# Optimization experiments

Measured on AMD Instinct MI355X. Metric: run time of the kernel, lower is better.

Reference implementation:

```python
import jax, jax.numpy as jnp
import numpy as np

B, N, IN_DIM, D, P, C = 256, 2048, 2, 128, 2048, 10
LN_EPS = 1e-5
NORM_EPS = 1e-12


def setup_inputs() -> dict:
    key = jax.random.key(0)
    ks = jax.random.split(key, 9)
    X = jax.random.normal(ks[0], (B, N, IN_DIM), dtype=jnp.float32)
    # deterministic pair subsample (stands in for torch.combinations + randperm[:max_pairs])
    rng = np.random.default_rng(0)
    i = rng.integers(0, N, size=(P,))
    j = rng.integers(0, N, size=(P,))
    j = np.where(i == j, (j + 1) % N, j)  # i != j, as combinations(r=2) guarantees
    pairs = jnp.asarray(np.stack([np.minimum(i, j), np.maximum(i, j)], axis=1), dtype=jnp.int32)
    # proj: Linear(2, D) + LayerNorm(D) (+ ReLU)
    W1 = jax.random.normal(ks[1], (IN_DIM, D), dtype=jnp.float32) / jnp.sqrt(jnp.float32(IN_DIM))
    b1 = jnp.zeros((D,), jnp.float32)
    gamma = jnp.ones((D,), jnp.float32)
    beta = jnp.zeros((D,), jnp.float32)
    # mlp: Linear(D, D) -> ReLU -> Linear(D, C)
    Wm1 = jax.random.normal(ks[2], (D, D), dtype=jnp.float32) / jnp.sqrt(jnp.float32(D))
    bm1 = jnp.zeros((D,), jnp.float32)
    Wm2 = jax.random.normal(ks[3], (D, C), dtype=jnp.float32) / jnp.sqrt(jnp.float32(D))
    bm2 = jnp.zeros((C,), jnp.float32)
    # frozen sdi_memory: row-normalized gaussian [C, D]
    mem = jax.random.normal(ks[4], (C, D), dtype=jnp.float32)
    mem = mem / jnp.maximum(jnp.linalg.norm(mem, axis=1, keepdims=True), NORM_EPS)
    return {"X": X, "pairs": pairs, "W1": W1, "b1": b1, "gamma": gamma, "beta": beta,
            "Wm1": Wm1, "bm1": bm1, "Wm2": Wm2, "bm2": bm2, "mem": mem}


def reference(X, pairs, W1, b1, gamma, beta, Wm1, bm1, Wm2, bm2, mem):
    # proj: Linear + LayerNorm (biased var, like torch) + ReLU  -> z: [B, N, D]
    h = jnp.einsum('bni,id->bnd', X, W1) + b1
    mu = h.mean(-1, keepdims=True)
    var = ((h - mu) ** 2).mean(-1, keepdims=True)
    z = jax.nn.relu(gamma * (h - mu) * jax.lax.rsqrt(var + LN_EPS) + beta)
    # pairwise gather: diffs then sums, concatenated along pair axis -> [B, 2P, D]
    za = z[:, pairs[:, 0], :]
    zb = z[:, pairs[:, 1], :]
    feats = jnp.concatenate([za - zb, za + zb], axis=1)
    # row-wise L2 normalize (F.normalize, eps=1e-12), then mean over pairs -> sdi: [B, D]
    feats = feats / jnp.maximum(jnp.linalg.norm(feats, axis=-1, keepdims=True), NORM_EPS)
    sdi = feats.mean(axis=1)
    # logits = sdi @ mem.T + mlp(sdi)
    logits = sdi @ mem.T + (jax.nn.relu(sdi @ Wm1 + bm1) @ Wm2 + bm2)
    return logits, sdi
```

## Files before the change

### kernel.cpp

```cpp
#include <hip/hip_runtime.h>

#define B 256
#define N 2048
#define P 2048
#define C 10
#define S_CHUNKS 8
#define PPB (P / S_CHUNKS)
#define NIT (PPB / 32)
#define LN_EPS 1e-5f

typedef float v2f __attribute__((ext_vector_type(2)));
typedef _Float16 h2 __attribute__((ext_vector_type(2)));

static __device__ __forceinline__ float fdot2(h2 a, h2 b, float c) {
#if __has_builtin(__builtin_amdgcn_fdot2)
    return __builtin_amdgcn_fdot2(a, b, c, false);
#else
    return (float)a.x * (float)b.x + (float)a.y * (float)b.y + c;
#endif
}
static __device__ __forceinline__ h2 h2fma(h2 a, h2 b, h2 c) {
#if __has_builtin(__builtin_elementwise_fma)
    return __builtin_elementwise_fma(a, b, c);
#else
    return a * b + c;
#endif
}
static __device__ __forceinline__ h2 h2relu(h2 x) {
#if __has_builtin(__builtin_elementwise_max)
    return __builtin_elementwise_max(x, h2{(_Float16)0.f, (_Float16)0.f});
#else
    h2 r;
    r.x = x.x > (_Float16)0.f ? x.x : (_Float16)0.f;
    r.y = x.y > (_Float16)0.f ? x.y : (_Float16)0.f;
    return r;
#endif
}
static __device__ __forceinline__ h2 pkrtz(float a, float b) {
#if __has_builtin(__builtin_amdgcn_cvt_pkrtz)
    return __builtin_bit_cast(h2, __builtin_amdgcn_cvt_pkrtz(a, b));
#else
    return h2{(_Float16)a, (_Float16)b};
#endif
}
static __device__ __forceinline__ unsigned pk_rne(float a, float b) {
    return __builtin_bit_cast(unsigned, h2{(_Float16)a, (_Float16)b});
}

static __device__ __forceinline__ float red16(float x) {
    x += __int_as_float(__builtin_amdgcn_update_dpp(0, __float_as_int(x), 0xB1,  0xF, 0xF, true));
    x += __int_as_float(__builtin_amdgcn_update_dpp(0, __float_as_int(x), 0x4E,  0xF, 0xF, true));
    x += __int_as_float(__builtin_amdgcn_update_dpp(0, __float_as_int(x), 0x141, 0xF, 0xF, true));
    x += __int_as_float(__builtin_amdgcn_update_dpp(0, __float_as_int(x), 0x140, 0xF, 0xF, true));
    return x;
}

__global__ __launch_bounds__(256) void triple_kernel(
        const float* __restrict__ X,
        const float* __restrict__ W1, const float* __restrict__ b1,
        const float* __restrict__ gamma, const float* __restrict__ beta,
        unsigned* __restrict__ wsw, uint2* __restrict__ T) {
    const int t = threadIdx.x;
    __shared__ float r[6][128];
    __shared__ float sc[6];

    float w0 = 0.f, w1 = 0.f, bb = 0.f;
    if (t < 128) {
        w0 = W1[t]; w1 = W1[128 + t]; bb = b1[t];
        r[0][t] = w0; r[1][t] = w1; r[2][t] = bb;
    }
    __syncthreads();
    for (int s = 64; s > 0; s >>= 1) {
        if (t < s) { r[0][t] += r[0][t + s]; r[1][t] += r[1][t + s]; r[2][t] += r[2][t + s]; }
        __syncthreads();
    }
    const float m0 = r[0][0] * (1.f / 128.f);
    const float m1 = r[1][0] * (1.f / 128.f);
    const float mb = r[2][0] * (1.f / 128.f);
    __syncthreads();
    float c0 = 0.f, c1 = 0.f, cb = 0.f;
    if (t < 128) {
        c0 = w0 - m0; c1 = w1 - m1; cb = bb - mb;
        r[0][t] = c0 * c0; r[1][t] = c1 * c1; r[2][t] = cb * cb;
        r[3][t] = c0 * c1; r[4][t] = c0 * cb; r[5][t] = c1 * cb;
    }
    __syncthreads();
    for (int s = 64; s > 0; s >>= 1) {
        if (t < s) {
            #pragma unroll
            for (int q = 0; q < 6; ++q) r[q][t] += r[q][t + s];
        }
        __syncthreads();
    }
    if (t < 6) sc[t] = r[t][0] * (1.f / 128.f);
    __syncthreads();

    const float S00 = sc[0], S11 = sc[1], Sbb = sc[2];
    const float S01 = sc[3], S0b = sc[4], S1b = sc[5];

    if (t < 128) {
        const float g = gamma[t];
        r[0][t] = g * c0; r[1][t] = g * c1; r[2][t] = g * cb; r[3][t] = beta[t];
    }
    __syncthreads();
    if (blockIdx.x == 0 && t < 16) {
        uint4* dst = (uint4*)wsw + t * 4;
        #pragma unroll
        for (int m = 0; m < 4; ++m) {
            const int d0 = t + 32 * m, d1 = d0 + 16;
            dst[m] = uint4{pk_rne(r[0][d0], r[0][d1]), pk_rne(r[1][d0], r[1][d1]),
                           pk_rne(r[2][d0], r[2][d1]), pk_rne(r[3][d0], r[3][d1])};
        }
    }

    const int gid = blockIdx.x * 256 + t;
    const float2 x = ((const float2*)X)[gid];
    const float v = fmaf(x.x * x.x, S00, fmaf(x.y * x.y, S11, Sbb))
                  + 2.f * fmaf(x.x * x.y, S01, fmaf(x.x, S0b, x.y * S1b));
    const float rs = rsqrtf(v + LN_EPS);
    T[gid] = uint2{pk_rne(rs * x.x, rs * x.y), pk_rne(rs, 1.f)};
}

__global__ __launch_bounds__(256) void pair_kernel(
        const uint2*    __restrict__ T,
        const int*      __restrict__ pairs,
        const unsigned* __restrict__ wsw,
        float* __restrict__ part) {
    const int b = blockIdx.x;
    const int chunk = blockIdx.y;
    const int tid = threadIdx.x;
    const int w = tid >> 6, l = tid & 63, g = l >> 4, s = l & 15;
    const int slot = w * 4 + g;

    __shared__ __align__(16) float lds[4096];
    uint2* Tl = (uint2*)lds;

    {
        const uint4* Tb4 = (const uint4*)(T + (size_t)b * N);
        uint4* Tl4 = (uint4*)lds;
        #pragma unroll
        for (int q = 0; q < 4; ++q) Tl4[q * 256 + tid] = Tb4[q * 256 + tid];
    }

    const uint4* Wl = (const uint4*)wsw + s * 4;
    h2 gw0[4], gw1[4], gbc[4], be2[4];
    #pragma unroll
    for (int m = 0; m < 4; ++m) {
        const uint4 wm = Wl[m];
        gw0[m] = __builtin_bit_cast(h2, wm.x);
        gw1[m] = __builtin_bit_cast(h2, wm.y);
        gbc[m] = __builtin_bit_cast(h2, wm.z);
        be2[m] = __builtin_bit_cast(h2, wm.w);
    }

    const int4* pr4 = (const int4*)pairs;
    const int i4base = chunk * (PPB / 2);

    v2f acc[4];
    #pragma unroll
    for (int m = 0; m < 4; ++m) acc[m] = v2f{0.f, 0.f};

    auto proc = [&](const uint2 ti, const uint2 tj) {
        const h2 abi = __builtin_bit_cast(h2, ti.x), ci = __builtin_bit_cast(h2, ti.y);
        const h2 abj = __builtin_bit_cast(h2, tj.x), cj = __builtin_bit_cast(h2, tj.y);
        const h2 aai = h2{abi.x, abi.x}, bbi = h2{abi.y, abi.y}, cci = h2{ci.x, ci.x};
        const h2 aaj = h2{abj.x, abj.x}, bbj = h2{abj.y, abj.y}, ccj = h2{cj.x, cj.x};
        h2 uu[4], vv[4];
        float nu0 = 0.f, nu1 = 0.f, nv0 = 0.f, nv1 = 0.f;
        #pragma unroll
        for (int m = 0; m < 4; ++m) {
            const h2 hi = h2relu(h2fma(aai, gw0[m], h2fma(bbi, gw1[m], h2fma(cci, gbc[m], be2[m]))));
            const h2 hj = h2relu(h2fma(aaj, gw0[m], h2fma(bbj, gw1[m], h2fma(ccj, gbc[m], be2[m]))));
            const h2 u = hi - hj;
            const h2 v = hi + hj;
            if (m & 1) { nu1 = fdot2(u, u, nu1); nv1 = fdot2(v, v, nv1); }
            else       { nu0 = fdot2(u, u, nu0); nv0 = fdot2(v, v, nv0); }
            uu[m] = u; vv[m] = v;
        }
        const float nu = red16(nu0 + nu1);
        const float nv = red16(nv0 + nv1);
        const float ru = rsqrtf(fmaxf(nu, 1e-24f));
        const float rv = rsqrtf(fmaxf(nv, 1e-24f));
        const h2 ruv = pkrtz(ru, rv);
        #pragma unroll
        for (int m = 0; m < 4; ++m) {
            acc[m].x = fdot2(h2{uu[m].x, vv[m].x}, ruv, acc[m].x);
            acc[m].y = fdot2(h2{uu[m].y, vv[m].y}, ruv, acc[m].y);
        }
    };

    const int4 idx0 = pr4[i4base + slot];
    __syncthreads();
    int4 idxN = pr4[i4base + 16 + slot];
    uint2 tiA = Tl[idx0.x], tjA = Tl[idx0.y];
    uint2 tiB = Tl[idx0.z], tjB = Tl[idx0.w];

    for (int t = 0; t < NIT; ++t) {
        const uint2 ntiA = Tl[idxN.x], ntjA = Tl[idxN.y];
        const uint2 ntiB = Tl[idxN.z], ntjB = Tl[idxN.w];
        const int t2 = (t + 2 < NIT) ? (t + 2) : (NIT - 1);
        const int4 idxNN = pr4[i4base + t2 * 16 + slot];

        proc(tiA, tjA);
        proc(tiB, tjB);

        tiA = ntiA; tjA = ntjA; tiB = ntiB; tjB = ntjB;
        idxN = idxNN;
    }

    __syncthreads();

    #pragma unroll
    for (int m = 0; m < 4; ++m) {
        lds[slot * 136 + (2 * m)     * 17 + s] = acc[m].x;
        lds[slot * 136 + (2 * m + 1) * 17 + s] = acc[m].y;
    }
    __syncthreads();
    if (tid < 128) {
        const int ss = tid & 15, kk = tid >> 4;
        float sum = 0.f;
        #pragma unroll
        for (int q = 0; q < 16; ++q) sum += lds[q * 136 + kk * 17 + ss];
        part[((size_t)b * S_CHUNKS + chunk) * 128 + tid] = sum;
    }
}

__global__ __launch_bounds__(256) void head_kernel(
        const float* __restrict__ part,
        const float* __restrict__ Wm1, const float* __restrict__ bm1,
        const float* __restrict__ Wm2, const float* __restrict__ bm2,
        const float* __restrict__ mem,
        float* __restrict__ out_logits, float* __restrict__ out_sdi) {
    const int b = blockIdx.x;
    const int t = threadIdx.x;
    __shared__ float s[128];
    __shared__ float h[128];

    if (t < 128) {
        float sv = 0.f;
        #pragma unroll
        for (int k = 0; k < S_CHUNKS; ++k)
            sv += part[((size_t)b * S_CHUNKS + k) * 128 + t];
        sv *= (1.f / (2.f * P));
        s[t] = sv;
        out_sdi[(size_t)b * 128 + t] = sv;
    }
    __syncthreads();
    if (t < 128) {
        float a = bm1[t];
        for (int d = 0; d < 128; ++d) a = fmaf(s[d], Wm1[d * 128 + t], a);
        h[t] = fmaxf(a, 0.f);
    }
    __syncthreads();
    if (t < 16 * C) {
        const int c = t >> 4, l = t & 15;
        float lg = 0.f;
        #pragma unroll
        for (int q = 0; q < 8; ++q) {
            const int d = l + 16 * q;
            lg = fmaf(s[d], mem[c * 128 + d], fmaf(h[d], Wm2[d * C + c], lg));
        }
        lg = red16(lg);
        if (l == 0) out_logits[(size_t)b * C + c] = lg + bm2[c];
    }
}

extern "C" void kernel_launch(void* const* d_in, const int* in_sizes, int n_in,
                              void* d_out, int out_size, void* d_ws, size_t ws_size,
                              hipStream_t stream) {
    const float* X     = (const float*)d_in[0];
    const int*   pairs = (const int*)  d_in[1];
    const float* W1    = (const float*)d_in[2];
    const float* b1    = (const float*)d_in[3];
    const float* gamma = (const float*)d_in[4];
    const float* beta  = (const float*)d_in[5];
    const float* Wm1   = (const float*)d_in[6];
    const float* bm1   = (const float*)d_in[7];
    const float* Wm2   = (const float*)d_in[8];
    const float* bm2   = (const float*)d_in[9];
    const float* mem   = (const float*)d_in[10];

    float* out = (float*)d_out;
    float* ws  = (float*)d_ws;
    unsigned* wsw  = (unsigned*)ws;
    uint2*    T    = (uint2*)(ws + 512);
    float*    part = ws + 512 + (size_t)B * N * 2;

    triple_kernel<<<(B * N) / 256, 256, 0, stream>>>(X, W1, b1, gamma, beta, wsw, T);
    pair_kernel<<<dim3(B, S_CHUNKS), 256, 0, stream>>>(T, pairs, wsw, part);
    head_kernel<<<B, 256, 0, stream>>>(part, Wm1, bm1, Wm2, bm2, mem,
                                       out, out + (size_t)B * C);
}
```

Before: 36.73 us.

## Fuse LayerNorm triple computation into pair kernel and halve pair chunks

The separate kernel that built per-point LayerNorm triples in global memory is removed. Each pair block now computes the weight statistics with wave shuffles, builds its batch row's triples directly into LDS from X, and converts the gamma-scaled weights to fp16 locally. This drops one kernel launch and the global write and read of the intermediate T buffer. In exchange every chunk block redoes the statistics and the per-point transform for its batch, so S_CHUNKS is cut from 8 to 4 to limit that duplicated work. That also halves the grid and lengthens each block's serial loop.

```diff
diff --git a/kernel.cpp b/kernel.cpp
--- a/kernel.cpp
+++ b/kernel.cpp
@@ -4,7 +4,7 @@
 #define N 2048
 #define P 2048
 #define C 10
-#define S_CHUNKS 8
+#define S_CHUNKS 4
 #define PPB (P / S_CHUNKS)
 #define NIT (PPB / 32)
 #define LN_EPS 1e-5f
@@ -55,76 +55,11 @@
     return x;
 }
 
-__global__ __launch_bounds__(256) void triple_kernel(
+__global__ __launch_bounds__(256) void fused_kernel(
         const float* __restrict__ X,
         const float* __restrict__ W1, const float* __restrict__ b1,
         const float* __restrict__ gamma, const float* __restrict__ beta,
-        unsigned* __restrict__ wsw, uint2* __restrict__ T) {
-    const int t = threadIdx.x;
-    __shared__ float r[6][128];
-    __shared__ float sc[6];
-
-    float w0 = 0.f, w1 = 0.f, bb = 0.f;
-    if (t < 128) {
-        w0 = W1[t]; w1 = W1[128 + t]; bb = b1[t];
-        r[0][t] = w0; r[1][t] = w1; r[2][t] = bb;
-    }
-    __syncthreads();
-    for (int s = 64; s > 0; s >>= 1) {
-        if (t < s) { r[0][t] += r[0][t + s]; r[1][t] += r[1][t + s]; r[2][t] += r[2][t + s]; }
-        __syncthreads();
-    }
-    const float m0 = r[0][0] * (1.f / 128.f);
-    const float m1 = r[1][0] * (1.f / 128.f);
-    const float mb = r[2][0] * (1.f / 128.f);
-    __syncthreads();
-    float c0 = 0.f, c1 = 0.f, cb = 0.f;
-    if (t < 128) {
-        c0 = w0 - m0; c1 = w1 - m1; cb = bb - mb;
-        r[0][t] = c0 * c0; r[1][t] = c1 * c1; r[2][t] = cb * cb;
-        r[3][t] = c0 * c1; r[4][t] = c0 * cb; r[5][t] = c1 * cb;
-    }
-    __syncthreads();
-    for (int s = 64; s > 0; s >>= 1) {
-        if (t < s) {
-            #pragma unroll
-            for (int q = 0; q < 6; ++q) r[q][t] += r[q][t + s];
-        }
-        __syncthreads();
-    }
-    if (t < 6) sc[t] = r[t][0] * (1.f / 128.f);
-    __syncthreads();
-
-    const float S00 = sc[0], S11 = sc[1], Sbb = sc[2];
-    const float S01 = sc[3], S0b = sc[4], S1b = sc[5];
-
-    if (t < 128) {
-        const float g = gamma[t];
-        r[0][t] = g * c0; r[1][t] = g * c1; r[2][t] = g * cb; r[3][t] = beta[t];
-    }
-    __syncthreads();
-    if (blockIdx.x == 0 && t < 16) {
-        uint4* dst = (uint4*)wsw + t * 4;
-        #pragma unroll
-        for (int m = 0; m < 4; ++m) {
-            const int d0 = t + 32 * m, d1 = d0 + 16;
-            dst[m] = uint4{pk_rne(r[0][d0], r[0][d1]), pk_rne(r[1][d0], r[1][d1]),
-                           pk_rne(r[2][d0], r[2][d1]), pk_rne(r[3][d0], r[3][d1])};
-        }
-    }
-
-    const int gid = blockIdx.x * 256 + t;
-    const float2 x = ((const float2*)X)[gid];
-    const float v = fmaf(x.x * x.x, S00, fmaf(x.y * x.y, S11, Sbb))
-                  + 2.f * fmaf(x.x * x.y, S01, fmaf(x.x, S0b, x.y * S1b));
-    const float rs = rsqrtf(v + LN_EPS);
-    T[gid] = uint2{pk_rne(rs * x.x, rs * x.y), pk_rne(rs, 1.f)};
-}
-
-__global__ __launch_bounds__(256) void pair_kernel(
-        const uint2*    __restrict__ T,
-        const int*      __restrict__ pairs,
-        const unsigned* __restrict__ wsw,
+        const int*   __restrict__ pairs,
         float* __restrict__ part) {
     const int b = blockIdx.x;
     const int chunk = blockIdx.y;
@@ -133,24 +68,74 @@
     const int slot = w * 4 + g;
 
     __shared__ __align__(16) float lds[4096];
+    __shared__ float wf[4][128];
+    __shared__ float sc[9];
     uint2* Tl = (uint2*)lds;
 
+    if (w == 0) {
+        const float w0a = W1[l],       w0b = W1[l + 64];
+        const float w1a = W1[128 + l], w1b = W1[128 + l + 64];
+        const float bba = b1[l],       bbb = b1[l + 64];
+        float s0 = w0a + w0b, s1 = w1a + w1b, sb = bba + bbb;
+        #pragma unroll
+        for (int m = 1; m < 64; m <<= 1) {
+            s0 += __shfl_xor(s0, m);
+            s1 += __shfl_xor(s1, m);
+            sb += __shfl_xor(sb, m);
+        }
+        const float m0 = s0 * (1.f / 128.f);
+        const float m1 = s1 * (1.f / 128.f);
+        const float mb = sb * (1.f / 128.f);
+        const float c0a = w0a - m0, c0b = w0b - m0;
+        const float c1a = w1a - m1, c1b = w1b - m1;
+        const float cba = bba - mb, cbb = bbb - mb;
+        float q[6] = { c0a*c0a + c0b*c0b, c1a*c1a + c1b*c1b, cba*cba + cbb*cbb,
+                       c0a*c1a + c0b*c1b, c0a*cba + c0b*cbb, c1a*cba + c1b*cbb };
+        #pragma unroll
+        for (int m = 1; m < 64; m <<= 1) {
+            #pragma unroll
+            for (int k = 0; k < 6; ++k) q[k] += __shfl_xor(q[k], m);
+        }
+        if (l < 6) sc[l] = q[l] * (1.f / 128.f);
+        if (l == 6) sc[6] = m0;
+        if (l == 7) sc[7] = m1;
+        if (l == 8) sc[8] = mb;
+    }
+    __syncthreads();
+
+    if (tid < 128) {
+        const float m0 = sc[6], m1 = sc[7], mb = sc[8];
+        const float g_ = gamma[tid];
+        wf[0][tid] = g_ * (W1[tid] - m0);
+        wf[1][tid] = g_ * (W1[128 + tid] - m1);
+        wf[2][tid] = g_ * (b1[tid] - mb);
+        wf[3][tid] = beta[tid];
+    }
+
     {
-        const uint4* Tb4 = (const uint4*)(T + (size_t)b * N);
-        uint4* Tl4 = (uint4*)lds;
-        #pragma unroll
-        for (int q = 0; q < 4; ++q) Tl4[q * 256 + tid] = Tb4[q * 256 + tid];
-    }
-
-    const uint4* Wl = (const uint4*)wsw + s * 4;
+        const float S00 = sc[0], S11 = sc[1], Sbb = sc[2];
+        const float S01 = sc[3], S0b = sc[4], S1b = sc[5];
+        const float2* Xb = (const float2*)(X + (size_t)b * N * 2);
+        #pragma unroll
+        for (int q = 0; q < 8; ++q) {
+            const int n = q * 256 + tid;
+            const float2 x = Xb[n];
+            const float v = fmaf(x.x * x.x, S00, fmaf(x.y * x.y, S11, Sbb))
+                          + 2.f * fmaf(x.x * x.y, S01, fmaf(x.x, S0b, x.y * S1b));
+            const float rs = rsqrtf(v + LN_EPS);
+            Tl[n] = uint2{pk_rne(rs * x.x, rs * x.y), pk_rne(rs, 1.f)};
+        }
+    }
+    __syncthreads();
+
     h2 gw0[4], gw1[4], gbc[4], be2[4];
     #pragma unroll
     for (int m = 0; m < 4; ++m) {
-        const uint4 wm = Wl[m];
-        gw0[m] = __builtin_bit_cast(h2, wm.x);
-        gw1[m] = __builtin_bit_cast(h2, wm.y);
-        gbc[m] = __builtin_bit_cast(h2, wm.z);
-        be2[m] = __builtin_bit_cast(h2, wm.w);
+        const int d0 = s + 32 * m, d1 = d0 + 16;
+        gw0[m] = h2{(_Float16)wf[0][d0], (_Float16)wf[0][d1]};
+        gw1[m] = h2{(_Float16)wf[1][d0], (_Float16)wf[1][d1]};
+        gbc[m] = h2{(_Float16)wf[2][d0], (_Float16)wf[2][d1]};
+        be2[m] = h2{(_Float16)wf[3][d0], (_Float16)wf[3][d1]};
     }
 
     const int4* pr4 = (const int4*)pairs;
@@ -190,7 +175,6 @@
     };
 
     const int4 idx0 = pr4[i4base + slot];
-    __syncthreads();
     int4 idxN = pr4[i4base + 16 + slot];
     uint2 tiA = Tl[idx0.x], tjA = Tl[idx0.y];
     uint2 tiB = Tl[idx0.z], tjB = Tl[idx0.w];
@@ -281,13 +265,10 @@
     const float* mem   = (const float*)d_in[10];
 
     float* out = (float*)d_out;
-    float* ws  = (float*)d_ws;
-    unsigned* wsw  = (unsigned*)ws;
-    uint2*    T    = (uint2*)(ws + 512);
-    float*    part = ws + 512 + (size_t)B * N * 2;
-
-    triple_kernel<<<(B * N) / 256, 256, 0, stream>>>(X, W1, b1, gamma, beta, wsw, T);
-    pair_kernel<<<dim3(B, S_CHUNKS), 256, 0, stream>>>(T, pairs, wsw, part);
+    float* part = (float*)d_ws;
+
+    fused_kernel<<<dim3(B, S_CHUNKS), 256, 0, stream>>>(X, W1, b1, gamma, beta,
+                                                        pairs, part);
     head_kernel<<<B, 256, 0, stream>>>(part, Wm1, bm1, Wm2, bm2, mem,
                                        out, out + (size_t)B * C);
 }
```

Result: faster. 32.36 us, median of 2 (-11.9%).
